# Kernel optimization log

Hardware: AMD Instinct MI355X
Metric: run time of the kernel (lower is better)

The kernel has to match this reference:

```python
import jax, jax.numpy as jnp
import numpy as np

B, N, C_IN = 32, 1024, 128
F0, F1, F2 = 64, 64, 64
OUT = 10
RATIOS = (0.8, 0.8)
EPS = 1e-5


def setup_inputs() -> dict:
    key = jax.random.key(0)
    ks = jax.random.split(key, 16)
    N_nodes = jax.random.randint(ks[0], (B,), N // 2, N + 1)
    mask = (jnp.arange(N)[None, :] < N_nodes[:, None]).astype(jnp.float32)
    x = jax.random.normal(ks[1], (B, N, C_IN), dtype=jnp.float32)
    # sparse-ish symmetric binary adjacency restricted to valid nodes
    A = (jax.random.uniform(ks[2], (B, N, N)) < 0.02).astype(jnp.float32)
    A = jnp.maximum(A, jnp.swapaxes(A, 1, 2))
    A = A * mask[:, :, None] * mask[:, None, :]
    def lin(k, fi, fo):
        b = 1.0 / np.sqrt(fi)
        kw, kb = jax.random.split(k)
        return (jax.random.uniform(kw, (fi, fo), minval=-b, maxval=b),
                jax.random.uniform(kb, (fo,), minval=-b, maxval=b))
    W0, b0 = lin(ks[3], C_IN, F0)
    W1, b1 = lin(ks[4], F0, F1)
    W2, b2 = lin(ks[5], F1, F2)
    bp0 = 1.0 / np.sqrt(F0)
    p0 = jax.random.uniform(ks[6], (F0, 1), minval=-bp0, maxval=bp0)
    bp1 = 1.0 / np.sqrt(F1)
    p1 = jax.random.uniform(ks[7], (F1, 1), minval=-bp1, maxval=bp1)
    Wfc, bfc = lin(ks[8], F2, OUT)
    return {"x": x, "A": A, "mask": mask, "N_nodes": N_nodes,
            "W0": W0, "b0": b0, "W1": W1, "b1": b1, "W2": W2, "b2": b2,
            "p0": p0, "p1": p1, "Wfc": Wfc, "bfc": bfc}


def _gconv(x, A, W, b):
    # Kipf-Welling normalized Laplacian conv, batched dense
    n = A.shape[1]
    A_hat = A + jnp.eye(n, dtype=A.dtype)[None]
    D = (jnp.sum(A_hat, axis=1) + EPS) ** -0.5  # [B,N]
    L = D[:, :, None] * A_hat * D[:, None, :]
    h = jnp.einsum('bnm,bmc->bnc', L, x) @ W + b
    return jax.nn.relu(h)


def _pool(x, A, mask, N_nodes, p, ratio):
    Bc, Nc, C = x.shape
    y = (x.reshape(Bc * Nc, C) @ p).reshape(Bc, Nc)
    y = y / jnp.sqrt(jnp.sum(p ** 2))
    N_remove = (N_nodes.astype(jnp.float32) * (1.0 - ratio)).astype(N_nodes.dtype)
    # remove the N_remove lowest-scoring valid nodes per graph
    y_eff = jnp.where(mask > 0, y, jnp.inf)
    ranks = jnp.argsort(jnp.argsort(y_eff, axis=1), axis=1)  # ascending rank
    new_mask = mask * (ranks >= N_remove[:, None]).astype(mask.dtype)
    x = x * jnp.tanh(y)[:, :, None] * new_mask[:, :, None]
    A = new_mask[:, :, None] * A * new_mask[:, None, :]
    return x, A, new_mask, N_nodes - N_remove


def reference(x, A, mask, N_nodes, W0, b0, W1, b1, W2, b2, p0, p1, Wfc, bfc):
    x = _gconv(x, A, W0, b0)
    x, A, mask, N_nodes = _pool(x, A, mask, N_nodes, p0, RATIOS[0])
    x = _gconv(x, A, W1, b1)
    x, A, mask, N_nodes = _pool(x, A, mask, N_nodes, p1, RATIOS[1])
    x = _gconv(x, A, W2, b2)
    x = jnp.max(x, axis=1)  # global max pool over nodes [B,F2]
    return x @ Wfc + bfc
```

## Files before the change

### kernel.cpp

```cpp
#include <hip/hip_runtime.h>
#include <cstdint>
#include <cstddef>

#define BB 32
#define NN 1024
#define CIN 128
#define FF 64
#define NOUT 10
#define CAP 128
#define EPSV 1e-5f

__global__ __launch_bounds__(256) void k_front(const float* __restrict__ A,
                                               const float* __restrict__ x,
                                               const float* __restrict__ W0,
                                               unsigned short* __restrict__ adj,
                                               int* __restrict__ cnt,
                                               float* __restrict__ c1,
                                               float* __restrict__ c2,
                                               float* __restrict__ T) {
    extern __shared__ float smem[];
    int tid = threadIdx.x;
    if (blockIdx.x < 2048) {
        int b = blockIdx.x & 31;
        int cch = blockIdx.x >> 5;
        int row0 = (b << 10) + cch * 16;
        float* Wl = smem;
        float (*xl)[CIN + 1] = (float (*)[CIN + 1])(smem + CIN * 64);
        for (int t = tid; t < CIN * 64; t += 256) Wl[t] = W0[t];
        for (int t = tid; t < 16 * CIN; t += 256) {
            int rr = t >> 7, kk = t & 127;
            xl[rr][kk] = x[(size_t)(row0 + rr) * CIN + kk];
        }
        __syncthreads();
        int wave = tid >> 6, lane = tid & 63;
        int rsub = lane >> 4, f0 = (lane & 15) * 4;
        int r = wave * 4 + rsub;
        float4 acc = {0.f, 0.f, 0.f, 0.f};
        const float* xr = xl[r];
#pragma unroll 8
        for (int k = 0; k < CIN; ++k) {
            float xv = xr[k];
            float4 w4 = *(const float4*)&Wl[k * 64 + f0];
            acc.x += xv * w4.x; acc.y += xv * w4.y;
            acc.z += xv * w4.z; acc.w += xv * w4.w;
        }
        *(float4*)&T[(size_t)(row0 + r) * 64 + f0] = acc;
    } else {
        int wave = tid >> 6;
        int lane = tid & 63;
        int r = (blockIdx.x - 2048) * 4 + wave;
        const float4* Arow = (const float4*)(A + (size_t)r * NN);
        size_t base = (size_t)r * CAP;
        int c = 0;
        unsigned long long lt = (lane == 0) ? 0ULL : ((1ULL << lane) - 1ULL);
        for (int it = 0; it < 4; ++it) {
            float4 v = Arow[it * 64 + lane];
            int j0 = it * 256 + lane * 4;
            unsigned long long m0 = __ballot(v.x != 0.f);
            unsigned long long m1 = __ballot(v.y != 0.f);
            unsigned long long m2 = __ballot(v.z != 0.f);
            unsigned long long m3 = __ballot(v.w != 0.f);
            int before = __popcll(m0 & lt) + __popcll(m1 & lt) +
                         __popcll(m2 & lt) + __popcll(m3 & lt);
            int p = c + before;
            if (v.x != 0.f) { if (p < CAP) adj[base + p] = (unsigned short)(j0 + 0); ++p; }
            if (v.y != 0.f) { if (p < CAP) adj[base + p] = (unsigned short)(j0 + 1); ++p; }
            if (v.z != 0.f) { if (p < CAP) adj[base + p] = (unsigned short)(j0 + 2); ++p; }
            if (v.w != 0.f) { if (p < CAP) adj[base + p] = (unsigned short)(j0 + 3); ++p; }
            c += __popcll(m0) + __popcll(m1) + __popcll(m2) + __popcll(m3);
        }
        if (lane == 0) {
            cnt[r] = (c > CAP) ? CAP : c;
            float D = 1.0f / sqrtf((float)c + 1.0f + EPSV);
            c1[r] = D;
            c2[r] = D * D;
        }
    }
}

__global__ __launch_bounds__(256) void k_mid(const unsigned short* __restrict__ adj,
                                             const int* __restrict__ cnt,
                                             const float* __restrict__ nm,
                                             float* __restrict__ c1, float* __restrict__ c2,
                                             const float* __restrict__ Xin,
                                             const float* __restrict__ W,
                                             const float* __restrict__ y,
                                             float* __restrict__ T) {
    int tid = threadIdx.x;
    if (blockIdx.x < 2048) {
        __shared__ __align__(16) float Wl[64 * 64];
        __shared__ float xl[16][65];
        __shared__ float sscale[16];
        int b = blockIdx.x & 31;
        int cch = blockIdx.x >> 5;
        int row0 = (b << 10) + cch * 16;
        if (tid < 16) {
            int r = row0 + tid;
            sscale[tid] = tanhf(y[r]) * nm[r];
        }
        for (int t = tid; t < 64 * 64; t += 256) Wl[t] = W[t];
        __syncthreads();
        for (int t = tid; t < 16 * 64; t += 256) {
            int rr = t >> 6, kk = t & 63;
            xl[rr][kk] = Xin[(size_t)(row0 + rr) * 64 + kk] * sscale[rr];
        }
        __syncthreads();
        int wave = tid >> 6, lane = tid & 63;
        int rsub = lane >> 4, f0 = (lane & 15) * 4;
        int r = wave * 4 + rsub;
        float4 acc = {0.f, 0.f, 0.f, 0.f};
        const float* xr = xl[r];
#pragma unroll 8
        for (int k = 0; k < 64; ++k) {
            float xv = xr[k];
            float4 w4 = *(const float4*)&Wl[k * 64 + f0];
            acc.x += xv * w4.x; acc.y += xv * w4.y;
            acc.z += xv * w4.z; acc.w += xv * w4.w;
        }
        *(float4*)&T[(size_t)(row0 + r) * 64 + f0] = acc;
    } else {
        int wave = tid >> 6, lane = tid & 63;
        int r = (blockIdx.x - 2048) * 4 + wave;
        int b = r >> 10;
        const unsigned short* arow = adj + (size_t)r * CAP;
        const float* nmb = nm + (b << 10);
        int n = cnt[r];
        float s = 0.f;
        if (lane < n)      s  = nmb[arow[lane]];
        if (lane + 64 < n) s += nmb[arow[lane + 64]];
        for (int sh = 32; sh; sh >>= 1) s += __shfl_xor(s, sh, 64);
        if (lane == 0) {
            float m = nm[r];
            float D = 1.0f / sqrtf(m * s + 1.0f + EPSV);
            c1[r] = m * D;
            c2[r] = D * D;
        }
    }
}

__global__ __launch_bounds__(256) void k_spmm(const unsigned short* __restrict__ adj,
                                              const int* __restrict__ cnt,
                                              const float* __restrict__ c1,
                                              const float* __restrict__ c2,
                                              const float* __restrict__ T,
                                              const float* __restrict__ bias,
                                              float* __restrict__ X,
                                              const float* __restrict__ p,
                                              float* __restrict__ y) {
    __shared__ __align__(16) float c1s[NN];
    int b   = blockIdx.x & 31;
    int cch = blockIdx.x >> 5;
    int tid = threadIdx.x;
    ((float4*)c1s)[tid] = ((const float4*)(c1 + (b << 10)))[tid];
    __syncthreads();
    int wave = tid >> 6, lane = tid & 63;
    int r = (b << 10) + cch * 4 + wave;
    const unsigned short* arow = adj + (size_t)r * CAP;
    int n = cnt[r];
    const float* Tb = T + ((size_t)(b << 10) << 6);
    float acc0 = 0.f, acc1 = 0.f, acc2 = 0.f, acc3 = 0.f;
    int t = 0;
    for (; t + 4 <= n; t += 4) {
        ushort4 j4 = *(const ushort4*)(arow + t);
        acc0 += c1s[j4.x] * Tb[((int)j4.x << 6) + lane];
        acc1 += c1s[j4.y] * Tb[((int)j4.y << 6) + lane];
        acc2 += c1s[j4.z] * Tb[((int)j4.z << 6) + lane];
        acc3 += c1s[j4.w] * Tb[((int)j4.w << 6) + lane];
    }
    for (; t < n; ++t) {
        int j = arow[t];
        acc0 += c1s[j] * Tb[(j << 6) + lane];
    }
    float acc = (acc0 + acc1) + (acc2 + acc3);
    int rl = r & 1023;
    float o = c1s[rl] * acc + c2[r] * T[((size_t)r << 6) + lane] + bias[lane];
    o = fmaxf(o, 0.f);
    X[((size_t)r << 6) + lane] = o;
    if (p != nullptr) {
        float pv = p[lane];
        float a = o * pv;
        float pp = pv * pv;
        for (int s = 32; s; s >>= 1) {
            a += __shfl_xor(a, s, 64);
            pp += __shfl_xor(pp, s, 64);
        }
        if (lane == 0) y[r] = a / sqrtf(pp);
    }
}

__global__ __launch_bounds__(256) void k_rank(const float* __restrict__ y,
                                              const float* __restrict__ maskSrc,
                                              const int* __restrict__ nsrc,
                                              float* __restrict__ nmOut,
                                              int* __restrict__ ncur) {
    __shared__ __align__(16) float yv[NN];
    int b = blockIdx.x >> 4;
    int sub = blockIdx.x & 15;
    int tid = threadIdx.x;
    const float INF = __builtin_inff();
    {
        float4 v = ((const float4*)(y + (b << 10)))[tid];
        float4 m = ((const float4*)(maskSrc + (b << 10)))[tid];
        v.x = (m.x > 0.f) ? v.x : INF;
        v.y = (m.y > 0.f) ? v.y : INF;
        v.z = (m.z > 0.f) ? v.z : INF;
        v.w = (m.w > 0.f) ? v.w : INF;
        ((float4*)yv)[tid] = v;
    }
    int n = nsrc[b];
    const float RM = (float)(1.0 - 0.8);
    int nrem = (int)((float)n * RM);
    if (sub == 0 && tid == 0) ncur[b] = n - nrem;
    __syncthreads();
    int i = (sub << 6) + (tid >> 2);
    int q = tid & 3;
    float yi = yv[i];
    int rank = 0;
    if (yi < INF) {
        const float4* jbase = (const float4*)yv + (q << 6);
        int j0 = q << 8;
#pragma unroll 8
        for (int t = 0; t < 64; ++t) {
            float4 a = jbase[t];
            int j = j0 + t * 4;
            rank += (a.x < yi || (a.x == yi && j     < i)) ? 1 : 0;
            rank += (a.y < yi || (a.y == yi && j + 1 < i)) ? 1 : 0;
            rank += (a.z < yi || (a.z == yi && j + 2 < i)) ? 1 : 0;
            rank += (a.w < yi || (a.w == yi && j + 3 < i)) ? 1 : 0;
        }
    }
    rank += __shfl_xor(rank, 1, 64);
    rank += __shfl_xor(rank, 2, 64);
    if (q == 0) {
        float nmv = (yi < INF && rank >= nrem) ? 1.f : 0.f;
        nmOut[(b << 10) + i] = nmv;
    }
}

__global__ __launch_bounds__(256) void k_final(const float* __restrict__ X,
                                               const float* __restrict__ Wfc,
                                               const float* __restrict__ bfc,
                                               float* __restrict__ out) {
    __shared__ float red[4][64];
    __shared__ float gl[64];
    int b = blockIdx.x, tid = threadIdx.x;
    int f = tid & 63, c = tid >> 6;
    float m = 0.f;
    for (int i = c; i < NN; i += 4)
        m = fmaxf(m, X[(((size_t)(b << 10) + i) << 6) + f]);
    red[c][f] = m;
    __syncthreads();
    if (tid < 64)
        gl[tid] = fmaxf(fmaxf(red[0][tid], red[1][tid]), fmaxf(red[2][tid], red[3][tid]));
    __syncthreads();
    if (tid < NOUT) {
        float acc = bfc[tid];
        for (int k = 0; k < 64; ++k) acc += gl[k] * Wfc[k * NOUT + tid];
        out[b * NOUT + tid] = acc;
    }
}

extern "C" void kernel_launch(void* const* d_in, const int* in_sizes, int n_in,
                              void* d_out, int out_size, void* d_ws, size_t ws_size,
                              hipStream_t stream) {
    const float* x    = (const float*)d_in[0];
    const float* A    = (const float*)d_in[1];
    const float* mask = (const float*)d_in[2];
    const int*   Nn   = (const int*)d_in[3];
    const float* W0   = (const float*)d_in[4];
    const float* b0   = (const float*)d_in[5];
    const float* W1   = (const float*)d_in[6];
    const float* b1   = (const float*)d_in[7];
    const float* W2   = (const float*)d_in[8];
    const float* b2   = (const float*)d_in[9];
    const float* p0   = (const float*)d_in[10];
    const float* p1   = (const float*)d_in[11];
    const float* Wfc  = (const float*)d_in[12];
    const float* bfc  = (const float*)d_in[13];
    float* out = (float*)d_out;

    char* ws = (char*)d_ws;
    size_t off = 0;
    auto alloc = [&](size_t bytes) -> void* {
        void* p = ws + off;
        off = (off + bytes + 255) & ~(size_t)255;
        return p;
    };
    unsigned short* adj = (unsigned short*)alloc((size_t)BB * NN * CAP * 2);
    int*   cnt  = (int*)  alloc((size_t)BB * NN * 4);
    float* X    = (float*)alloc((size_t)BB * NN * 64 * 4);
    float* T    = (float*)alloc((size_t)BB * NN * 64 * 4);
    float* c1   = (float*)alloc((size_t)BB * NN * 4);
    float* c2   = (float*)alloc((size_t)BB * NN * 4);
    float* y    = (float*)alloc((size_t)BB * NN * 4);
    float* nm0  = (float*)alloc((size_t)BB * NN * 4);
    float* nm1  = (float*)alloc((size_t)BB * NN * 4);
    int*   nc0  = (int*)  alloc((size_t)BB * 4);
    int*   nc1  = (int*)  alloc((size_t)BB * 4);

    const int RW = BB * NN;
    const size_t frontLds = (size_t)(CIN * 64 + 16 * (CIN + 1)) * 4;
    k_front<<<2048 + RW / 4, 256, frontLds, stream>>>(A, x, W0, adj, cnt, c1, c2, T);
    k_spmm<<<RW / 4, 256, 0, stream>>>(adj, cnt, c1, c2, T, b0, X, p0, y);
    k_rank<<<BB * 16, 256, 0, stream>>>(y, mask, Nn, nm0, nc0);
    k_mid<<<2048 + RW / 4, 256, 0, stream>>>(adj, cnt, nm0, c1, c2, X, W1, y, T);
    k_spmm<<<RW / 4, 256, 0, stream>>>(adj, cnt, c1, c2, T, b1, X, p1, y);
    k_rank<<<BB * 16, 256, 0, stream>>>(y, nm0, nc0, nm1, nc1);
    k_mid<<<2048 + RW / 4, 256, 0, stream>>>(adj, cnt, nm1, c1, c2, X, W2, y, T);
    k_spmm<<<RW / 4, 256, 0, stream>>>(adj, cnt, c1, c2, T, b2, X, nullptr, nullptr);
    k_final<<<BB, 256, 0, stream>>>(X, Wfc, bfc, out);
}
```

Before: 395.2 us.

## Drop LDS staging in dense GEMM blocks, read weights and rows from global

The dense feature-transform blocks in k_front and k_mid no longer copy the weight matrix and input rows into shared memory. Each thread now reads float4 row chunks and weight rows straight from global memory (relying on cache hits) and applies the tanh/mask scale after the dot product instead of before. The adjacency-compaction path also issues all four row loads up front to get more loads in flight. This removes per-block LDS fill and barriers and frees LDS for occupancy, at the cost of more global/L2 traffic for the weights.

```diff
diff --git a/kernel.cpp b/kernel.cpp
--- a/kernel.cpp
+++ b/kernel.cpp
@@ -18,43 +18,45 @@
                                                float* __restrict__ c1,
                                                float* __restrict__ c2,
                                                float* __restrict__ T) {
-    extern __shared__ float smem[];
     int tid = threadIdx.x;
     if (blockIdx.x < 2048) {
         int b = blockIdx.x & 31;
         int cch = blockIdx.x >> 5;
         int row0 = (b << 10) + cch * 16;
-        float* Wl = smem;
-        float (*xl)[CIN + 1] = (float (*)[CIN + 1])(smem + CIN * 64);
-        for (int t = tid; t < CIN * 64; t += 256) Wl[t] = W0[t];
-        for (int t = tid; t < 16 * CIN; t += 256) {
-            int rr = t >> 7, kk = t & 127;
-            xl[rr][kk] = x[(size_t)(row0 + rr) * CIN + kk];
-        }
-        __syncthreads();
         int wave = tid >> 6, lane = tid & 63;
         int rsub = lane >> 4, f0 = (lane & 15) * 4;
-        int r = wave * 4 + rsub;
+        int r = row0 + wave * 4 + rsub;
+        const float4* xr = (const float4*)(x + (size_t)r * CIN);
         float4 acc = {0.f, 0.f, 0.f, 0.f};
-        const float* xr = xl[r];
-#pragma unroll 8
-        for (int k = 0; k < CIN; ++k) {
-            float xv = xr[k];
-            float4 w4 = *(const float4*)&Wl[k * 64 + f0];
-            acc.x += xv * w4.x; acc.y += xv * w4.y;
-            acc.z += xv * w4.z; acc.w += xv * w4.w;
-        }
-        *(float4*)&T[(size_t)(row0 + r) * 64 + f0] = acc;
+#pragma unroll 4
+        for (int k4 = 0; k4 < CIN / 4; ++k4) {
+            float4 xv = xr[k4];
+            float4 w0 = *(const float4*)&W0[(k4 * 4 + 0) * 64 + f0];
+            float4 w1 = *(const float4*)&W0[(k4 * 4 + 1) * 64 + f0];
+            float4 w2 = *(const float4*)&W0[(k4 * 4 + 2) * 64 + f0];
+            float4 w3 = *(const float4*)&W0[(k4 * 4 + 3) * 64 + f0];
+            acc.x += xv.x * w0.x; acc.y += xv.x * w0.y; acc.z += xv.x * w0.z; acc.w += xv.x * w0.w;
+            acc.x += xv.y * w1.x; acc.y += xv.y * w1.y; acc.z += xv.y * w1.z; acc.w += xv.y * w1.w;
+            acc.x += xv.z * w2.x; acc.y += xv.z * w2.y; acc.z += xv.z * w2.z; acc.w += xv.z * w2.w;
+            acc.x += xv.w * w3.x; acc.y += xv.w * w3.y; acc.z += xv.w * w3.z; acc.w += xv.w * w3.w;
+        }
+        *(float4*)&T[(size_t)r * 64 + f0] = acc;
     } else {
         int wave = tid >> 6;
         int lane = tid & 63;
         int r = (blockIdx.x - 2048) * 4 + wave;
         const float4* Arow = (const float4*)(A + (size_t)r * NN);
+        float4 v0 = Arow[lane];
+        float4 v1 = Arow[64 + lane];
+        float4 v2 = Arow[128 + lane];
+        float4 v3 = Arow[192 + lane];
         size_t base = (size_t)r * CAP;
         int c = 0;
         unsigned long long lt = (lane == 0) ? 0ULL : ((1ULL << lane) - 1ULL);
+        float4 vv[4] = {v0, v1, v2, v3};
+#pragma unroll
         for (int it = 0; it < 4; ++it) {
-            float4 v = Arow[it * 64 + lane];
+            float4 v = vv[it];
             int j0 = it * 256 + lane * 4;
             unsigned long long m0 = __ballot(v.x != 0.f);
             unsigned long long m1 = __ballot(v.y != 0.f);
@@ -88,36 +90,29 @@
                                              float* __restrict__ T) {
     int tid = threadIdx.x;
     if (blockIdx.x < 2048) {
-        __shared__ __align__(16) float Wl[64 * 64];
-        __shared__ float xl[16][65];
-        __shared__ float sscale[16];
         int b = blockIdx.x & 31;
         int cch = blockIdx.x >> 5;
         int row0 = (b << 10) + cch * 16;
-        if (tid < 16) {
-            int r = row0 + tid;
-            sscale[tid] = tanhf(y[r]) * nm[r];
-        }
-        for (int t = tid; t < 64 * 64; t += 256) Wl[t] = W[t];
-        __syncthreads();
-        for (int t = tid; t < 16 * 64; t += 256) {
-            int rr = t >> 6, kk = t & 63;
-            xl[rr][kk] = Xin[(size_t)(row0 + rr) * 64 + kk] * sscale[rr];
-        }
-        __syncthreads();
         int wave = tid >> 6, lane = tid & 63;
         int rsub = lane >> 4, f0 = (lane & 15) * 4;
-        int r = wave * 4 + rsub;
+        int r = row0 + wave * 4 + rsub;
+        float sc = tanhf(y[r]) * nm[r];
+        const float4* xr = (const float4*)(Xin + (size_t)r * 64);
         float4 acc = {0.f, 0.f, 0.f, 0.f};
-        const float* xr = xl[r];
-#pragma unroll 8
-        for (int k = 0; k < 64; ++k) {
-            float xv = xr[k];
-            float4 w4 = *(const float4*)&Wl[k * 64 + f0];
-            acc.x += xv * w4.x; acc.y += xv * w4.y;
-            acc.z += xv * w4.z; acc.w += xv * w4.w;
-        }
-        *(float4*)&T[(size_t)(row0 + r) * 64 + f0] = acc;
+#pragma unroll 4
+        for (int k4 = 0; k4 < 16; ++k4) {
+            float4 xv = xr[k4];
+            float4 w0 = *(const float4*)&W[(k4 * 4 + 0) * 64 + f0];
+            float4 w1 = *(const float4*)&W[(k4 * 4 + 1) * 64 + f0];
+            float4 w2 = *(const float4*)&W[(k4 * 4 + 2) * 64 + f0];
+            float4 w3 = *(const float4*)&W[(k4 * 4 + 3) * 64 + f0];
+            acc.x += xv.x * w0.x; acc.y += xv.x * w0.y; acc.z += xv.x * w0.z; acc.w += xv.x * w0.w;
+            acc.x += xv.y * w1.x; acc.y += xv.y * w1.y; acc.z += xv.y * w1.z; acc.w += xv.y * w1.w;
+            acc.x += xv.z * w2.x; acc.y += xv.z * w2.y; acc.z += xv.z * w2.z; acc.w += xv.z * w2.w;
+            acc.x += xv.w * w3.x; acc.y += xv.w * w3.y; acc.z += xv.w * w3.z; acc.w += xv.w * w3.w;
+        }
+        acc.x *= sc; acc.y *= sc; acc.z *= sc; acc.w *= sc;
+        *(float4*)&T[(size_t)r * 64 + f0] = acc;
     } else {
         int wave = tid >> 6, lane = tid & 63;
         int r = (blockIdx.x - 2048) * 4 + wave;
@@ -299,8 +294,7 @@
     int*   nc1  = (int*)  alloc((size_t)BB * 4);
 
     const int RW = BB * NN;
-    const size_t frontLds = (size_t)(CIN * 64 + 16 * (CIN + 1)) * 4;
-    k_front<<<2048 + RW / 4, 256, frontLds, stream>>>(A, x, W0, adj, cnt, c1, c2, T);
+    k_front<<<2048 + RW / 4, 256, 0, stream>>>(A, x, W0, adj, cnt, c1, c2, T);
     k_spmm<<<RW / 4, 256, 0, stream>>>(adj, cnt, c1, c2, T, b0, X, p0, y);
     k_rank<<<BB * 16, 256, 0, stream>>>(y, mask, Nn, nm0, nc0);
     k_mid<<<2048 + RW / 4, 256, 0, stream>>>(adj, cnt, nm0, c1, c2, X, W1, y, T);
```

New measurement: 422.3 us. 1.07x slower.
